# Kernel tuning notes

Hardware: AMD Instinct MI355X
Metric: run time of the kernel (lower is better)

The kernel has to match this reference:

```python
import jax, jax.numpy as jnp
import numpy as np


def _pool_mat(N, pn):
    # F.interpolate(mode='area') == adaptive_avg_pool1d: output i averages
    # input indices [floor(i*N/pn), ceil((i+1)*N/pn))
    W = np.zeros((pn, N), dtype=np.float32)
    for i in range(pn):
        s = (i * N) // pn
        e = -((-(i + 1) * N) // pn)  # ceil((i+1)*N/pn)
        W[i, s:e] = 1.0 / (e - s)
    return W


def _up_mat(pn, N):
    # F.interpolate(mode='linear', align_corners=False) from length pn to N
    W = np.zeros((N, pn), dtype=np.float32)
    scale = pn / N
    for j in range(N):
        pos = max((j + 0.5) * scale - 0.5, 0.0)
        i0 = min(int(np.floor(pos)), pn - 1)
        i1 = min(i0 + 1, pn - 1)
        frac = pos - i0
        W[j, i0] += 1.0 - frac
        W[j, i1] += frac
    return W


def setup_inputs() -> dict:
    key = jax.random.key(0)
    k1, k2 = jax.random.split(key)
    B, N, C, K = 512, 16, 256, 8192
    f = jax.random.normal(k1, (B, N, C), dtype=jnp.float32)
    # original init: uniform(-1/K, 1/K)
    emb = jax.random.uniform(k2, (K, C), dtype=jnp.float32, minval=-1.0 / K, maxval=1.0 / K)
    return {"f": f, "emb": emb}


def reference(f, emb):
    B, N, C = f.shape
    fT = jnp.transpose(f, (0, 2, 1))            # [B, C, N]
    f_ng = jax.lax.stop_gradient(fT)
    emb_ng = jax.lax.stop_gradient(emb)
    e_sq = jnp.sum(emb_ng * emb_ng, axis=1)     # [K]
    f_rest = f_ng
    f_hat = jnp.zeros_like(f_ng)
    commit = jnp.float32(0.0)
    qlat = jnp.float32(0.0)
    for pn in range(1, N + 1):
        rest_bcn = jax.lax.stop_gradient(f_rest)
        if pn < N:
            Wp = jnp.asarray(_pool_mat(N, pn))             # [pn, N]
            rest = jnp.einsum('pn,bcn->bpc', Wp, rest_bcn).reshape(-1, C)
        else:
            rest = jnp.transpose(rest_bcn, (0, 2, 1)).reshape(-1, C)
        # squared euclidean distances [B*pn, K]
        d = jnp.sum(rest * rest, axis=1, keepdims=True) + e_sq - 2.0 * (rest @ emb_ng.T)
        idx = jnp.argmin(d, axis=1).reshape(B, pn)
        h = jnp.transpose(emb[idx], (0, 2, 1))             # [B, C, pn]
        if pn < N:
            Wu = jnp.asarray(_up_mat(pn, N))               # [N, pn]
            h = jnp.einsum('np,bcp->bcn', Wu, h)
        f_hat = f_hat + h
        f_rest = f_rest - h
        commit = commit + 0.25 * jnp.mean((jax.lax.stop_gradient(f_hat) - fT) ** 2)
        qlat = qlat + jnp.mean((f_hat - f_ng) ** 2)
    commit = commit / N
    qlat = qlat / N
    # straight-through estimator
    f_hat_out = jax.lax.stop_gradient(f_hat) - f_ng + fT
    return jnp.transpose(f_hat_out, (0, 2, 1)), commit, qlat
```

## Files before the change

kernel.cpp:

```cpp
#include <hip/hip_runtime.h>
#include <math.h>

#define BB 512
#define NN 16
#define CC 256
#define KK 8192
#define BNC (BB*NN*CC)

typedef unsigned short u16;
typedef __attribute__((ext_vector_type(8))) short bf16x8;
typedef __attribute__((ext_vector_type(4))) float f32x4;

__device__ __forceinline__ u16 f2bf(float x) {
    unsigned u = __float_as_uint(x);
    unsigned r = (u + 0x7fffu + ((u >> 16) & 1u)) >> 16;
    return (u16)r;
}

__device__ __forceinline__ void gl2lds16(const void* g, void* l) {
    __builtin_amdgcn_global_load_lds(
        (const __attribute__((address_space(1))) void*)g,
        (__attribute__((address_space(3))) void*)l,
        16, 0, 0);
}

__global__ void esq_kernel(const float* __restrict__ emb, float* __restrict__ e_sq) {
    int gid  = blockIdx.x * blockDim.x + threadIdx.x;
    int wave = gid >> 6;
    int lane = gid & 63;
    const float4 v = *(const float4*)(emb + (size_t)wave * CC + lane * 4);
    float s = v.x*v.x + v.y*v.y + v.z*v.z + v.w*v.w;
    #pragma unroll
    for (int m = 32; m >= 1; m >>= 1) s += __shfl_xor(s, m, 64);
    if (lane == 0) e_sq[wave] = s;
}

__global__ void cvt_emb_kernel(const float* __restrict__ emb, u16* __restrict__ out) {
    int gid = blockIdx.x * blockDim.x + threadIdx.x;
    float4 v = ((const float4*)emb)[gid];
    ushort4 o;
    o.x = f2bf(v.x); o.y = f2bf(v.y); o.z = f2bf(v.z); o.w = f2bf(v.w);
    ((ushort4*)out)[gid] = o;
}

__global__ void init_pool_kernel(const float* __restrict__ f,
                                 u16* __restrict__ rest_bf) {
    int b = blockIdx.x;
    int c = threadIdx.x;
    const float* base = f + (size_t)b * NN * CC + c;
    float acc = 0.f;
    #pragma unroll
    for (int n = 0; n < NN; ++n) acc += base[(size_t)n * CC];
    rest_bf[(size_t)b * CC + c] = f2bf(acc * (1.0f / 16.0f));
}

__device__ __forceinline__ unsigned long long shfl_xor_u64(unsigned long long v, int m) {
    unsigned lo = (unsigned)v, hi = (unsigned)(v >> 32);
    lo = __shfl_xor(lo, m, 64);
    hi = __shfl_xor(hi, m, 64);
    return ((unsigned long long)hi << 32) | lo;
}

__global__ __launch_bounds__(256, 2) void dist_mfma_kernel(
        const u16* __restrict__ A, const u16* __restrict__ Bm,
        const float* __restrict__ e_sq,
        unsigned long long* __restrict__ packed, int cpb) {
    __shared__ __align__(16) u16 sA[16384];
    __shared__ __align__(16) u16 sB[16384];
    const int tid = threadIdx.x;
    const int w = tid >> 6, l = tid & 63;
    const int r0 = blockIdx.x * 64;
    const int c0 = blockIdx.y * cpb;
    const int ncb = cpb >> 8;
    const int arow = l & 15;
    const int aq   = l >> 4;

    {
        const int phys = tid & 31;
        #pragma unroll
        for (int i = 0; i < 8; ++i) {
            int s = tid + 256 * i;
            int row = s >> 5;
            int g = phys ^ (row & 31);
            gl2lds16(A + (((size_t)(r0 + row)) << 8) + g * 8,
                     (char*)sA + (size_t)(w * 64 + 256 * i) * 16);
        }
    }
    const int gsel = (l & 3) ^ ((l >> 2) & 3) ^ ((l >> 4) & 3);
    const int crow = l >> 2;

    #define STAGE_B(cb_, kc_, buf_)                                            \
        {                                                                      \
            const u16* src = Bm + (((size_t)(c0 + (cb_) * 256 + w * 64)) << 8) \
                             + (kc_) * 32 + gsel * 8;                          \
            char* dst = (char*)sB + ((w * 2 + (buf_)) << 12);                  \
            _Pragma("unroll")                                                  \
            for (int ld = 0; ld < 4; ++ld)                                     \
                gl2lds16(src + ((size_t)(crow + 16 * ld) << 8), dst + (ld << 10)); \
        }

    STAGE_B(0, 0, 0);
    __syncthreads();

    float bestd[16];
    int   bestk[16];
    #pragma unroll
    for (int t = 0; t < 16; ++t) { bestd[t] = 1e30f; bestk[t] = 0; }

    for (int cb = 0; cb < ncb; ++cb) {
        f32x4 acc[4][4];
        const f32x4 z = {0.f, 0.f, 0.f, 0.f};
        #pragma unroll
        for (int i = 0; i < 4; ++i)
            #pragma unroll
            for (int j = 0; j < 4; ++j) acc[i][j] = z;

        #pragma unroll
        for (int kc = 0; kc < 8; ++kc) {
            const int buf = kc & 1;
            __builtin_amdgcn_s_waitcnt(0x0F70);
            bf16x8 a[4], b[4];
            const u16* wb = sB + ((w * 2 + buf) << 11);
            #pragma unroll
            for (int t = 0; t < 4; ++t) {
                int row = t * 16 + arow;
                int g = kc * 4 + aq;
                int phys = g ^ (row & 31);
                a[t] = *(const bf16x8*)(sA + row * 256 + phys * 8);
                int cc_ = t * 16 + arow;
                int sig = cc_ * 4 + (aq ^ (cc_ & 3) ^ ((cc_ >> 2) & 3));
                b[t] = *(const bf16x8*)(wb + sig * 8);
            }
            int cbn = (kc == 7) ? ((cb + 1 < ncb) ? cb + 1 : cb) : cb;
            int kcn = (kc + 1) & 7;
            STAGE_B(cbn, kcn, buf ^ 1);
            #pragma unroll
            for (int i = 0; i < 4; ++i)
                #pragma unroll
                for (int j = 0; j < 4; ++j)
                    acc[i][j] = __builtin_amdgcn_mfma_f32_16x16x32_bf16(
                                    a[i], b[j], acc[i][j], 0, 0, 0);
        }

        float esq[4];
        #pragma unroll
        for (int j = 0; j < 4; ++j)
            esq[j] = e_sq[c0 + cb * 256 + w * 64 + j * 16 + arow];
        #pragma unroll
        for (int i = 0; i < 4; ++i)
            #pragma unroll
            for (int r = 0; r < 4; ++r) {
                const int slot = i * 4 + r;
                #pragma unroll
                for (int j = 0; j < 4; ++j) {
                    float d = fmaf(-2.0f, acc[i][j][r], esq[j]);
                    int k = c0 + cb * 256 + w * 64 + j * 16 + arow;
                    if (d < bestd[slot]) { bestd[slot] = d; bestk[slot] = k; }
                }
            }
    }

    #pragma unroll
    for (int t = 0; t < 16; ++t) {
        unsigned u = __float_as_uint(bestd[t]);
        u = (u & 0x80000000u) ? ~u : (u | 0x80000000u);
        unsigned long long p = ((unsigned long long)u << 32) | (unsigned)bestk[t];
        #pragma unroll
        for (int m = 1; m < 16; m <<= 1) {
            unsigned long long o = shfl_xor_u64(p, m);
            if (o < p) p = o;
        }
        if (arow == 0)
            atomicMin(&packed[r0 + (t >> 2) * 16 + aq * 4 + (t & 3)], p);
    }
    #undef STAGE_B
}

__global__ void update_pool_kernel(const float* __restrict__ f,
                                   const float* __restrict__ emb,
                                   const unsigned long long* __restrict__ packed,
                                   float* __restrict__ f_rest,
                                   float* __restrict__ f_hat,
                                   float* __restrict__ slots,
                                   u16* __restrict__ rest_bf, int pn) {
    int b = blockIdx.x;
    int c = threadIdx.x;
    __shared__ int sk[NN];
    __shared__ float red[4];
    if (threadIdx.x < pn)
        sk[threadIdx.x] = (int)(unsigned)(packed[b * pn + threadIdx.x] & 0xffffffffull);
    __syncthreads();

    float fr[NN];
    float acc_sq = 0.f;
    #pragma unroll
    for (int n = 0; n < NN; ++n) {
        double pos = (n + 0.5) * ((double)pn / 16.0) - 0.5;
        if (pos < 0.0) pos = 0.0;
        int i0 = (int)floor(pos);
        if (i0 > pn - 1) i0 = pn - 1;
        int i1 = i0 + 1;
        if (i1 > pn - 1) i1 = pn - 1;
        double frac = pos - (double)i0;
        float w1 = (float)frac;
        float w0 = (float)(1.0 - frac);
        float h = w0 * emb[(size_t)sk[i0] * CC + c] + w1 * emb[(size_t)sk[i1] * CC + c];
        size_t off = ((size_t)b * NN + n) * CC + c;
        float fh = f_hat[off] + h;
        f_hat[off] = fh;
        float fre = f_rest[off] - h;
        f_rest[off] = fre;
        fr[n] = fre;
        float diff = fh - f[off];
        acc_sq += diff * diff;
    }

    int wv = threadIdx.x >> 6, ln = threadIdx.x & 63;
    #pragma unroll
    for (int m = 32; m >= 1; m >>= 1) acc_sq += __shfl_xor(acc_sq, m, 64);
    if (ln == 0) red[wv] = acc_sq;

    int pn2 = pn + 1;
    if (pn < NN) {
        for (int p = 0; p < pn2; ++p) {
            int s = (p * NN) / pn2;
            int e = ((p + 1) * NN + pn2 - 1) / pn2;
            float v = 0.f;
            for (int n = s; n < e; ++n) v += fr[n];
            v *= 1.0f / (float)(e - s);
            rest_bf[((size_t)(b * pn2 + p)) * CC + c] = f2bf(v);
        }
    }
    __syncthreads();
    if (threadIdx.x == 0)
        atomicAdd(&slots[b & 255], (red[0] + red[1]) + (red[2] + red[3]));
}

__global__ void final_kernel(const float* __restrict__ slots, float* __restrict__ out_scalars) {
    float v = slots[threadIdx.x];
    #pragma unroll
    for (int m = 32; m >= 1; m >>= 1) v += __shfl_xor(v, m, 64);
    __shared__ float red[4];
    int wv = threadIdx.x >> 6, ln = threadIdx.x & 63;
    if (ln == 0) red[wv] = v;
    __syncthreads();
    if (threadIdx.x == 0) {
        float S = (red[0] + red[1]) + (red[2] + red[3]);
        float qlat = S / (float)BNC / (float)NN;
        out_scalars[0] = 0.25f * qlat;
        out_scalars[1] = qlat;
    }
}

extern "C" void kernel_launch(void* const* d_in, const int* in_sizes, int n_in,
                              void* d_out, int out_size, void* d_ws, size_t ws_size,
                              hipStream_t stream) {
    (void)in_sizes; (void)n_in; (void)out_size; (void)ws_size;
    const float* f   = (const float*)d_in[0];
    const float* emb = (const float*)d_in[1];
    float* out = (float*)d_out;

    float* ws      = (float*)d_ws;
    float* f_rest  = ws;
    float* r2_pad  = f_rest + BNC;
    float* e_sq    = r2_pad + BB * NN;
    float* slots   = e_sq + KK;
    unsigned long long* packed_all = (unsigned long long*)(slots + 256);
    u16* rest_bf = (u16*)(packed_all + (size_t)BB * 136);
    u16* emb_bf  = rest_bf + (size_t)BB * NN * CC;

    float* f_hat = out;

    hipMemsetAsync(out, 0, (size_t)BNC * sizeof(float), stream);
    hipMemcpyAsync(f_rest, f, (size_t)BNC * sizeof(float), hipMemcpyDeviceToDevice, stream);
    hipMemsetAsync(slots, 0, 256 * sizeof(float), stream);
    hipMemsetAsync(packed_all, 0xFF, (size_t)BB * 136 * sizeof(unsigned long long), stream);
    esq_kernel<<<KK / 4, 256, 0, stream>>>(emb, e_sq);
    cvt_emb_kernel<<<KK * CC / 4 / 256, 256, 0, stream>>>(emb, emb_bf);
    init_pool_kernel<<<BB, 256, 0, stream>>>(f, rest_bf);

    static const int splits_tab[17] = {0,32,32,16,16,8,8,8,8,4,4,4,4,4,4,4,4};

    for (int pn = 1; pn <= NN; ++pn) {
        unsigned long long* packed = packed_all + (size_t)BB * (pn * (pn - 1) / 2);
        int splits = splits_tab[pn];
        int cpb = KK / splits;
        dim3 grid(BB * pn / 64, splits);
        dist_mfma_kernel<<<grid, 256, 0, stream>>>(rest_bf, emb_bf, e_sq, packed, cpb);
        update_pool_kernel<<<BB, 256, 0, stream>>>(f, emb, packed, f_rest, f_hat,
                                                   slots, rest_bf, pn);
    }
    final_kernel<<<1, 256, 0, stream>>>(slots, out + BNC);
}
```

Before: 820.5 us.

## Load codebook fragments directly into registers instead of staging through LDS

The distance kernel no longer stages codebook tiles into shared memory with async global-to-LDS copies. Each wave now loads its B fragments straight from global memory into registers, using a one-step register double buffer (bcur/bnxt) to prefetch the next k-chunk. This removes the shared-memory B buffer, its waitcnt synchronisation and the LDS reads, and may raise occupancy. In exchange, global loads are less coalesced (16-byte per-lane strided rows) and latency is hidden only by a single prefetch.

Measured after the change: 1.337 ms. 63.0% more time.

```diff
diff --git a/kernel.cpp b/kernel.cpp
--- a/kernel.cpp
+++ b/kernel.cpp
@@ -66,7 +66,6 @@
         const float* __restrict__ e_sq,
         unsigned long long* __restrict__ packed, int cpb) {
     __shared__ __align__(16) u16 sA[16384];
-    __shared__ __align__(16) u16 sB[16384];
     const int tid = threadIdx.x;
     const int w = tid >> 6, l = tid & 63;
     const int r0 = blockIdx.x * 64;
@@ -86,20 +85,15 @@
                      (char*)sA + (size_t)(w * 64 + 256 * i) * 16);
         }
     }
-    const int gsel = (l & 3) ^ ((l >> 2) & 3) ^ ((l >> 4) & 3);
-    const int crow = l >> 2;
-
-    #define STAGE_B(cb_, kc_, buf_)                                            \
-        {                                                                      \
-            const u16* src = Bm + (((size_t)(c0 + (cb_) * 256 + w * 64)) << 8) \
-                             + (kc_) * 32 + gsel * 8;                          \
-            char* dst = (char*)sB + ((w * 2 + (buf_)) << 12);                  \
-            _Pragma("unroll")                                                  \
-            for (int ld = 0; ld < 4; ++ld)                                     \
-                gl2lds16(src + ((size_t)(crow + 16 * ld) << 8), dst + (ld << 10)); \
-        }
-
-    STAGE_B(0, 0, 0);
+
+    const u16* bp = Bm + (((size_t)(c0 + w * 64 + arow)) << 8) + (aq << 3);
+    const float* ep = e_sq + c0 + w * 64 + arow;
+
+    bf16x8 bcur[4], bnxt[4];
+    #pragma unroll
+    for (int t = 0; t < 4; ++t)
+        bcur[t] = *(const bf16x8*)(bp + t * 4096);
+
     __syncthreads();
 
     float bestd[16];
@@ -108,6 +102,10 @@
     for (int t = 0; t < 16; ++t) { bestd[t] = 1e30f; bestk[t] = 0; }
 
     for (int cb = 0; cb < ncb; ++cb) {
+        float esq[4];
+        #pragma unroll
+        for (int j = 0; j < 4; ++j) esq[j] = ep[cb * 256 + j * 16];
+
         f32x4 acc[4][4];
         const f32x4 z = {0.f, 0.f, 0.f, 0.f};
         #pragma unroll
@@ -115,37 +113,32 @@
             #pragma unroll
             for (int j = 0; j < 4; ++j) acc[i][j] = z;
 
+        const bool lastcb = (cb == ncb - 1);
         #pragma unroll
         for (int kc = 0; kc < 8; ++kc) {
-            const int buf = kc & 1;
-            __builtin_amdgcn_s_waitcnt(0x0F70);
-            bf16x8 a[4], b[4];
-            const u16* wb = sB + ((w * 2 + buf) << 11);
+            size_t noff = (kc < 7) ? (size_t)((kc + 1) * 32)
+                                   : (lastcb ? (size_t)(kc * 32) : (size_t)65536);
+            #pragma unroll
+            for (int t = 0; t < 4; ++t)
+                bnxt[t] = *(const bf16x8*)(bp + noff + t * 4096);
+
+            bf16x8 a[4];
             #pragma unroll
             for (int t = 0; t < 4; ++t) {
                 int row = t * 16 + arow;
-                int g = kc * 4 + aq;
-                int phys = g ^ (row & 31);
-                a[t] = *(const bf16x8*)(sA + row * 256 + phys * 8);
-                int cc_ = t * 16 + arow;
-                int sig = cc_ * 4 + (aq ^ (cc_ & 3) ^ ((cc_ >> 2) & 3));
-                b[t] = *(const bf16x8*)(wb + sig * 8);
+                a[t] = *(const bf16x8*)(sA + row * 256 + (((kc * 4 + aq) ^ (row & 31)) << 3));
             }
-            int cbn = (kc == 7) ? ((cb + 1 < ncb) ? cb + 1 : cb) : cb;
-            int kcn = (kc + 1) & 7;
-            STAGE_B(cbn, kcn, buf ^ 1);
             #pragma unroll
             for (int i = 0; i < 4; ++i)
                 #pragma unroll
                 for (int j = 0; j < 4; ++j)
                     acc[i][j] = __builtin_amdgcn_mfma_f32_16x16x32_bf16(
-                                    a[i], b[j], acc[i][j], 0, 0, 0);
-        }
-
-        float esq[4];
-        #pragma unroll
-        for (int j = 0; j < 4; ++j)
-            esq[j] = e_sq[c0 + cb * 256 + w * 64 + j * 16 + arow];
+                                    a[i], bcur[j], acc[i][j], 0, 0, 0);
+            #pragma unroll
+            for (int t = 0; t < 4; ++t) bcur[t] = bnxt[t];
+        }
+        bp += 65536;
+
         #pragma unroll
         for (int i = 0; i < 4; ++i)
             #pragma unroll
@@ -173,7 +166,6 @@
         if (arow == 0)
             atomicMin(&packed[r0 + (t >> 2) * 16 + aq * 4 + (t & 3)], p);
     }
-    #undef STAGE_B
 }
 
 __global__ void update_pool_kernel(const float* __restrict__ f,
```
